# Optimization experiments

Hardware: AMD Instinct MI355X
Metric: run time of the kernel (lower is better)

The kernel has to match this reference:

```python
import jax, jax.numpy as jnp
import numpy as np

NUM_CLASS = 20
ALPHA = 1.0
BETA = 1.0
IGNORE = 255


def _fdiff(f, ax):
    """np.gradient/torch.gradient with unit spacing along axis ax (edge_order=1)."""
    n = f.shape[ax]
    sl = lambda a, b: jax.lax.slice_in_dim(f, a, b, axis=ax)
    interior = (sl(2, n) - sl(0, n - 2)) * 0.5
    first = sl(1, 2) - sl(0, 1)
    last = sl(n - 1, n) - sl(n - 2, n - 1)
    return jnp.concatenate([first, interior, last], axis=ax)


def _lga(targets):
    # one-hot over all classes at once: [C, B, D, H, W]
    cls = jnp.arange(NUM_CLASS, dtype=targets.dtype)[:, None, None, None, None]
    oh = (targets[None] == cls).astype(jnp.float32)
    res = jnp.zeros(targets.shape, jnp.float32)
    for ax in (2, 3, 4):  # spatial dims of [C,B,D,H,W]
        res = res + jnp.sum(jnp.abs(_fdiff(oh, ax)), axis=0)
    return res  # [B, D, H, W]


def setup_inputs() -> dict:
    key = jax.random.key(0)
    k1, k2, k3, k4 = jax.random.split(key, 4)
    B, D, H, W = 1, 256, 256, 32
    predictions = jax.random.normal(k1, (B, NUM_CLASS, D, H, W), dtype=jnp.float32)
    targets = jax.random.randint(k2, (B, D, H, W), 0, NUM_CLASS)
    ignore = jax.random.uniform(k3, (B, D, H, W)) < 0.02
    targets = jnp.where(ignore, IGNORE, targets).astype(jnp.int32)
    class_weights = jax.random.uniform(k4, (NUM_CLASS,), dtype=jnp.float32) + 0.1
    return {"predictions": predictions, "targets": targets, "class_weights": class_weights}


def reference(predictions, targets, class_weights):
    targets = targets.astype(jnp.int32)
    valid = targets != IGNORE
    t = jnp.where(valid, targets, 0)
    # weighted CE, reduction='none': -w[t] * log_softmax(pred)[t], 0 at ignore
    logp = jax.nn.log_softmax(predictions, axis=1)
    logp_t = jnp.take_along_axis(logp, t[:, None], axis=1)[:, 0]  # [B,D,H,W]
    w = class_weights[t]
    loss = jnp.where(valid, -w * logp_t, 0.0)
    lga_weights = ALPHA + BETA * _lga(targets)
    num = jnp.sum(loss * lga_weights)
    den = jnp.sum(jnp.where(valid, w, 0.0))
    return num / den
```

## Files before the change

### kernel.cpp

```cpp
#include <hip/hip_runtime.h>

#define NUM_CLASS 20
#define IGNORE_V 255
#define WW 32
#define HH 256
#define DDEPTH 256
#define NVOX (DDEPTH * HH * WW)
#define CHUNK 1024
#define NBLK (NVOX / CHUNK)
#define HALF 10

__device__ __forceinline__ float fpair(int a, int b) {
    return (a == b) ? 0.0f : ((a == IGNORE_V || b == IGNORE_V) ? 1.0f : 2.0f);
}

__device__ __forceinline__ void stage16(const float* gsrc, float* ldst) {
    __builtin_amdgcn_global_load_lds(
        (const __attribute__((address_space(1))) void*)gsrc,
        (__attribute__((address_space(3))) void*)ldst,
        16, 0, 0);
}

__global__ __launch_bounds__(256) void pal_main(
    const float* __restrict__ pred,
    const int*   __restrict__ tgt,
    const float* __restrict__ cw,
    float2*      __restrict__ partial)
{
    __shared__ __align__(16) float lbuf[HALF * CHUNK];
    __shared__ float lcw[NUM_CLASS];
    if (threadIdx.x < NUM_CLASS) lcw[threadIdx.x] = cw[threadIdx.x];

    const int tid   = threadIdx.x;
    const int lane  = tid & 63;
    const int wid   = tid >> 6;
    const int base  = blockIdx.x * CHUNK;
    const int v0    = base + tid * 4;
    const int w0    = v0 & (WW - 1);
    const int h     = (v0 >> 5) & (HH - 1);
    const int d     = v0 >> 13;

    const int4 t4 = *reinterpret_cast<const int4*>(tgt + v0);
    const int t[4] = {t4.x, t4.y, t4.z, t4.w};
    const int tm1 = tgt[v0 - ((w0 != 0) ? 1 : 0)];
    const int tp4 = tgt[v0 + 3 + ((w0 != WW - 4) ? 1 : 0)];
    const int4 tu4 = *reinterpret_cast<const int4*>(tgt + v0 - ((h != 0)          ? WW      : 0));
    const int4 td4 = *reinterpret_cast<const int4*>(tgt + v0 + ((h != HH - 1)     ? WW      : 0));
    const int4 tb4 = *reinterpret_cast<const int4*>(tgt + v0 - ((d != 0)          ? WW * HH : 0));
    const int4 tf4 = *reinterpret_cast<const int4*>(tgt + v0 + ((d != DDEPTH - 1) ? WW * HH : 0));

    const int woff = wid * 256;
    const float* gwave = pred + base + woff + lane * 4;
    float s[4]  = {0.f, 0.f, 0.f, 0.f};
    float pt[4] = {0.f, 0.f, 0.f, 0.f};

    #pragma unroll
    for (int ph = 0; ph < 2; ph++) {
        const int cs = ph * HALF;
        #pragma unroll
        for (int k = 0; k < HALF; k++)
            stage16(gwave + (size_t)(cs + k) * NVOX, lbuf + k * CHUNK + woff);
        __syncthreads();

        const float* lp = lbuf + tid * 4;
        #pragma unroll
        for (int k = 0; k < HALF; k++) {
            const float4 x = *reinterpret_cast<const float4*>(lp + k * CHUNK);
            const int c = cs + k;
            const float xx[4] = {x.x, x.y, x.z, x.w};
            #pragma unroll
            for (int j = 0; j < 4; j++) {
                s[j] += __expf(xx[j]);
                if (t[j] == c) pt[j] = xx[j];
            }
        }
        __syncthreads();
    }

    const int tu[4] = {tu4.x, tu4.y, tu4.z, tu4.w};
    const int td[4] = {td4.x, td4.y, td4.z, td4.w};
    const int tb[4] = {tb4.x, tb4.y, tb4.z, tb4.w};
    const int tf[4] = {tf4.x, tf4.y, tf4.z, tf4.w};
    const float scH = (h == 0 || h == HH - 1)     ? 1.0f : 0.5f;
    const float scD = (d == 0 || d == DDEPTH - 1) ? 1.0f : 0.5f;

    float num = 0.0f, den = 0.0f;
    #pragma unroll
    for (int j = 0; j < 4; j++) {
        const int tj = t[j];
        if (tj != IGNORE_V) {
            const int wj = w0 + j;
            const int tL = (j > 0) ? t[j-1] : ((w0 == 0)      ? t[0] : tm1);
            const int tR = (j < 3) ? t[j+1] : ((w0 == WW - 4) ? t[3] : tp4);
            const float scW = (wj == 0 || wj == WW - 1) ? 1.0f : 0.5f;
            const float lga = scW * fpair(tL, tR)
                            + scH * fpair(tu[j], td[j])
                            + scD * fpair(tb[j], tf[j]);
            const float wt = lcw[tj];
            num += wt * (__logf(s[j]) - pt[j]) * (1.0f + lga);
            den += wt;
        }
    }

    #pragma unroll
    for (int off = 32; off > 0; off >>= 1) {
        num += __shfl_down(num, off);
        den += __shfl_down(den, off);
    }
    __shared__ float sn[4], sd[4];
    if (lane == 0) { sn[wid] = num; sd[wid] = den; }
    __syncthreads();
    if (tid == 0)
        partial[blockIdx.x] = make_float2((sn[0] + sn[1]) + (sn[2] + sn[3]),
                                          (sd[0] + sd[1]) + (sd[2] + sd[3]));
}

__global__ __launch_bounds__(256) void pal_final(
    const float2* __restrict__ partial, float* __restrict__ out)
{
    const float4* p4 = reinterpret_cast<const float4*>(partial);
    float num = 0.f, den = 0.f;
    #pragma unroll
    for (int k = 0; k < 4; k++) {
        const float4 f = p4[threadIdx.x + 256 * k];
        num += f.x + f.z;
        den += f.y + f.w;
    }
    #pragma unroll
    for (int off = 32; off > 0; off >>= 1) {
        num += __shfl_down(num, off);
        den += __shfl_down(den, off);
    }
    __shared__ float sn[4], sd[4];
    const int lane = threadIdx.x & 63;
    const int wid  = threadIdx.x >> 6;
    if (lane == 0) { sn[wid] = num; sd[wid] = den; }
    __syncthreads();
    if (threadIdx.x == 0)
        out[0] = ((sn[0] + sn[1]) + (sn[2] + sn[3])) /
                 ((sd[0] + sd[1]) + (sd[2] + sd[3]));
}

extern "C" void kernel_launch(void* const* d_in, const int* in_sizes, int n_in,
                              void* d_out, int out_size, void* d_ws, size_t ws_size,
                              hipStream_t stream) {
    const float* pred = (const float*)d_in[0];
    const int*   tgt  = (const int*)d_in[1];
    const float* cw   = (const float*)d_in[2];
    float*  out     = (float*)d_out;
    float2* partial = (float2*)d_ws;

    pal_main<<<NBLK, 256, 0, stream>>>(pred, tgt, cw, partial);
    pal_final<<<1, 256, 0, stream>>>(partial, out);
}
```

Measured before the change: 241.9 us.

## Double-buffer per-wave LDS staging with vmcnt waits instead of block barriers

Splits the 20 prediction classes into four groups of five and stages them into per-wave double buffers in LDS. Explicit s_waitcnt vmcnt/lgkmcnt waits replace the block-wide __syncthreads, so each wave computes on one buffer while the next group's global loads are in flight. The aim is to hide memory latency and remove barrier stalls in this bandwidth-bound kernel. It relies on in-order vmcnt accounting and hand-placed waits, which is fragile if the compiler reorders or adds memory operations.

```diff
diff --git a/kernel.cpp b/kernel.cpp
--- a/kernel.cpp
+++ b/kernel.cpp
@@ -8,7 +8,9 @@
 #define NVOX (DDEPTH * HH * WW)
 #define CHUNK 1024
 #define NBLK (NVOX / CHUNK)
-#define HALF 10
+
+#define WAITVM(N)  asm volatile("s_waitcnt vmcnt(" #N ")" ::: "memory")
+#define WAITLGKM0  asm volatile("s_waitcnt lgkmcnt(0)" ::: "memory")
 
 __device__ __forceinline__ float fpair(int a, int b) {
     return (a == b) ? 0.0f : ((a == IGNORE_V || b == IGNORE_V) ? 1.0f : 2.0f);
@@ -27,46 +29,39 @@
     const float* __restrict__ cw,
     float2*      __restrict__ partial)
 {
-    __shared__ __align__(16) float lbuf[HALF * CHUNK];
+    __shared__ __align__(16) float lbuf[4][2][5][256];
     __shared__ float lcw[NUM_CLASS];
     if (threadIdx.x < NUM_CLASS) lcw[threadIdx.x] = cw[threadIdx.x];
+    __syncthreads();
 
-    const int tid   = threadIdx.x;
-    const int lane  = tid & 63;
-    const int wid   = tid >> 6;
-    const int base  = blockIdx.x * CHUNK;
-    const int v0    = base + tid * 4;
-    const int w0    = v0 & (WW - 1);
-    const int h     = (v0 >> 5) & (HH - 1);
-    const int d     = v0 >> 13;
+    const int tid  = threadIdx.x;
+    const int lane = tid & 63;
+    const int wid  = tid >> 6;
+    const int base = blockIdx.x * CHUNK;
+    const int v0   = base + tid * 4;
+    const int w0   = v0 & (WW - 1);
+    const int h    = (v0 >> 5) & (HH - 1);
+    const int d    = v0 >> 13;
 
-    const int4 t4 = *reinterpret_cast<const int4*>(tgt + v0);
-    const int t[4] = {t4.x, t4.y, t4.z, t4.w};
-    const int tm1 = tgt[v0 - ((w0 != 0) ? 1 : 0)];
-    const int tp4 = tgt[v0 + 3 + ((w0 != WW - 4) ? 1 : 0)];
+    const int4 t4  = *reinterpret_cast<const int4*>(tgt + v0);
+    const int tm1  = tgt[v0 - ((w0 != 0) ? 1 : 0)];
+    const int tp4  = tgt[v0 + 3 + ((w0 != WW - 4) ? 1 : 0)];
     const int4 tu4 = *reinterpret_cast<const int4*>(tgt + v0 - ((h != 0)          ? WW      : 0));
     const int4 td4 = *reinterpret_cast<const int4*>(tgt + v0 + ((h != HH - 1)     ? WW      : 0));
     const int4 tb4 = *reinterpret_cast<const int4*>(tgt + v0 - ((d != 0)          ? WW * HH : 0));
     const int4 tf4 = *reinterpret_cast<const int4*>(tgt + v0 + ((d != DDEPTH - 1) ? WW * HH : 0));
 
-    const int woff = wid * 256;
-    const float* gwave = pred + base + woff + lane * 4;
+    const int t[4] = {t4.x, t4.y, t4.z, t4.w};
+    const float* gw = pred + base + wid * 256 + lane * 4;
+
     float s[4]  = {0.f, 0.f, 0.f, 0.f};
     float pt[4] = {0.f, 0.f, 0.f, 0.f};
 
-    #pragma unroll
-    for (int ph = 0; ph < 2; ph++) {
-        const int cs = ph * HALF;
+    auto consume = [&](int b, int c0) {
         #pragma unroll
-        for (int k = 0; k < HALF; k++)
-            stage16(gwave + (size_t)(cs + k) * NVOX, lbuf + k * CHUNK + woff);
-        __syncthreads();
-
-        const float* lp = lbuf + tid * 4;
-        #pragma unroll
-        for (int k = 0; k < HALF; k++) {
-            const float4 x = *reinterpret_cast<const float4*>(lp + k * CHUNK);
-            const int c = cs + k;
+        for (int k = 0; k < 5; k++) {
+            const float4 x = *reinterpret_cast<const float4*>(&lbuf[wid][b][k][lane * 4]);
+            const int c = c0 + k;
             const float xx[4] = {x.x, x.y, x.z, x.w};
             #pragma unroll
             for (int j = 0; j < 4; j++) {
@@ -74,8 +69,21 @@
                 if (t[j] == c) pt[j] = xx[j];
             }
         }
-        __syncthreads();
-    }
+        WAITLGKM0;
+    };
+
+    #pragma unroll
+    for (int k = 0; k < 5; k++) stage16(gw + (size_t)k        * NVOX, &lbuf[wid][0][k][0]);
+    #pragma unroll
+    for (int k = 0; k < 5; k++) stage16(gw + (size_t)(5 + k)  * NVOX, &lbuf[wid][1][k][0]);
+    WAITVM(5);  consume(0, 0);
+    #pragma unroll
+    for (int k = 0; k < 5; k++) stage16(gw + (size_t)(10 + k) * NVOX, &lbuf[wid][0][k][0]);
+    WAITVM(5);  consume(1, 5);
+    #pragma unroll
+    for (int k = 0; k < 5; k++) stage16(gw + (size_t)(15 + k) * NVOX, &lbuf[wid][1][k][0]);
+    WAITVM(5);  consume(0, 10);
+    WAITVM(0);  consume(1, 15);
 
     const int tu[4] = {tu4.x, tu4.y, tu4.z, tu4.w};
     const int td[4] = {td4.x, td4.y, td4.z, td4.w};
```

New measurement: 247.7 us. 1.02x slower.
